# Optimization experiments

Hardware: AMD Instinct MI355X
Metric: run time of the kernel (lower is better)

## Reference

```python
import jax, jax.numpy as jnp
import numpy as np

NEG_INF = -1.0e12  # matches torch's -1000000000000.0 fill


def setup_inputs() -> dict:
    key = jax.random.key(0)
    k1, k2, k3, k4, k5 = jax.random.split(key, 5)
    B, S, H, D = 4, 4096, 1024, 64  # D = hidden_size // num_attention_heads
    x = jax.random.normal(k1, (B, S, H), dtype=jnp.float32)
    mask = jax.random.randint(k2, (B, S), 0, 2, dtype=jnp.int32)
    # nn.Linear(H, D, bias=False) weights have shape [D, H]; y = x @ W.T
    scale = 1.0 / np.sqrt(H)
    Wk = jax.random.normal(k3, (D, H), dtype=jnp.float32) * scale
    Wq = jax.random.normal(k4, (D, H), dtype=jnp.float32) * scale
    Wv = jax.random.normal(k5, (D, H), dtype=jnp.float32) * scale
    return {"x": x, "mask": mask, "Wk": Wk, "Wq": Wq, "Wv": Wv}


def reference(x, mask, Wk, Wq, Wv):
    D = Wk.shape[0]
    scale = 1.0 / jnp.sqrt(jnp.asarray(D, dtype=x.dtype))
    keys = jnp.einsum('bsh,dh->bsd', x, Wk)      # [B,S,D]
    queries = jnp.einsum('bsh,dh->bsd', x, Wq)   # [B,S,D]
    # NOTE: original computes keys @ queries^T (K first), scores[b,i,j] = k_i . q_j
    scores = jnp.einsum('bsd,btd->bst', keys, queries) * scale  # [B,S,S]
    # mask==0 at position p masks COLUMN p of scores (dim=2), matching
    # attention_scores[batch_idx, :, position_idx] = -1e12
    scores = jnp.where((mask == 0)[:, None, :], NEG_INF, scores)
    weights = jax.nn.softmax(scores, axis=2)
    # dropout prob = 0.0 -> identity
    values = jnp.einsum('bsh,dh->bsd', x, Wv)    # [B,S,D]
    hidden_state = jnp.einsum('bst,btd->bsd', weights, values)
    return hidden_state
```

## Files before the change

kernel.cpp:

```cpp
#include <hip/hip_runtime.h>
#include <hip/hip_bf16.h>
#include <math.h>

#define B_ 4
#define S_ 4096
#define H_ 1024
#define D_ 64
#define M_ (B_*S_)
#define NEGINF (-1.0e12f)

typedef __attribute__((ext_vector_type(8))) short bf16x8;
typedef __attribute__((ext_vector_type(8))) unsigned short u16x8;
typedef __attribute__((ext_vector_type(8))) _Float16 f16x8;
typedef __attribute__((ext_vector_type(4))) _Float16 f16x4;
typedef __attribute__((ext_vector_type(4))) float f32x4;

#define OFF_WH   0
#define OFF_WL   393216
#define OFF_KF   786432
#define OFF_QF   2883584
#define OFF_VTF  4980736
#define OFF_PACC 7077888
#define OFF_PM   23855104
#define OFF_PL2  24117248

__device__ __forceinline__ unsigned short f2bf_rne(float f) {
    union { float f; unsigned u; } v; v.f = f;
    unsigned r = (v.u + 0x7fffu + ((v.u >> 16) & 1u)) >> 16;
    return (unsigned short)r;
}
__device__ __forceinline__ float bf2f(unsigned short h) {
    union { unsigned u; float f; } v; v.u = ((unsigned)h) << 16;
    return v.f;
}
__device__ __forceinline__ void split1(float f, unsigned short& h, unsigned short& l) {
    union { float f; unsigned u; } v; v.f = f;
    h = (unsigned short)(v.u >> 16);
    l = f2bf_rne(f - bf2f(h));
}
__device__ __forceinline__ void split8(const float4& a, const float4& b, u16x8& hi, u16x8& lo) {
    float f[8] = {a.x,a.y,a.z,a.w, b.x,b.y,b.z,b.w};
    #pragma unroll
    for (int i = 0; i < 8; ++i) {
        unsigned short h, l; split1(f[i], h, l);
        hi[i] = h; lo[i] = l;
    }
}

__global__ __launch_bounds__(256)
void wconv(const float* __restrict__ Wk, const float* __restrict__ Wq,
           const float* __restrict__ Wv, char* __restrict__ wsb)
{
    short* Wh = (short*)(wsb + OFF_WH);
    short* Wl = (short*)(wsb + OFF_WL);
    const int n = blockIdx.x;
    const int t = threadIdx.x;
    const float* src = (n < 64) ? (Wk + (size_t)n*H_)
                     : (n < 128 ? (Wq + (size_t)(n-64)*H_) : (Wv + (size_t)(n-128)*H_));
    float4 v = *(const float4*)(src + t*4);
    unsigned short h0,l0,h1,l1,h2,l2,h3,l3;
    split1(v.x,h0,l0); split1(v.y,h1,l1); split1(v.z,h2,l2); split1(v.w,h3,l3);
    ushort4 hv; hv.x=h0; hv.y=h1; hv.z=h2; hv.w=h3;
    ushort4 lv; lv.x=l0; lv.y=l1; lv.z=l2; lv.w=l3;
    *(ushort4*)(Wh + n*1024 + t*4) = hv;
    *(ushort4*)(Wl + n*1024 + t*4) = lv;
}

__global__ __launch_bounds__(256, 1)
void qkv_mfma(const float* __restrict__ x, char* __restrict__ wsb)
{
    __shared__ short Ah[4096], Al[4096];
    __shared__ short Bh[12288], Bl[12288];

    const short* __restrict__ Whg = (const short*)(wsb + OFF_WH);
    const short* __restrict__ Wlg = (const short*)(wsb + OFF_WL);
    _Float16* Kf  = (_Float16*)(wsb + OFF_KF);
    _Float16* Qf  = (_Float16*)(wsb + OFF_QF);
    _Float16* Vtf = (_Float16*)(wsb + OFF_VTF);

    const int tid = threadIdx.x;
    const int w = tid >> 6, l = tid & 63;
    const int l15 = l & 15, l4 = l >> 4;
    const int m0 = blockIdx.x * 64;

    const int arow0 = tid >> 3,        ac0 = (tid & 7) * 8;
    const int arow1 = (tid + 256) >> 3;
    const int aoff0 = arow0*64 + (ac0 ^ ((arow0 & 7) << 3));
    const int aoff1 = arow1*64 + (ac0 ^ ((arow1 & 7) << 3));

    float4 xa0, xa1, xa2, xa3;
    u16x8 wbh0, wbh1, wbh2, wbh3, wbh4, wbh5;
    u16x8 wbl0, wbl1, wbl2, wbl3, wbl4, wbl5;

#define QKV_PREFETCH(K0) do {                                                  \
    xa0 = *(const float4*)(x + (size_t)(m0 + arow0)*H_ + (K0) + ac0);          \
    xa1 = *(const float4*)(x + (size_t)(m0 + arow0)*H_ + (K0) + ac0 + 4);      \
    xa2 = *(const float4*)(x + (size_t)(m0 + arow1)*H_ + (K0) + ac0);          \
    xa3 = *(const float4*)(x + (size_t)(m0 + arow1)*H_ + (K0) + ac0 + 4);      \
    { int idx=tid;        int r=idx>>3, c8=(idx&7)*8;                          \
      wbh0 = *(const u16x8*)(Whg + r*1024 + (K0) + c8);                        \
      wbl0 = *(const u16x8*)(Wlg + r*1024 + (K0) + c8); }                      \
    { int idx=tid+256;    int r=idx>>3, c8=(idx&7)*8;                          \
      wbh1 = *(const u16x8*)(Whg + r*1024 + (K0) + c8);                        \
      wbl1 = *(const u16x8*)(Wlg + r*1024 + (K0) + c8); }                      \
    { int idx=tid+512;    int r=idx>>3, c8=(idx&7)*8;                          \
      wbh2 = *(const u16x8*)(Whg + r*1024 + (K0) + c8);                        \
      wbl2 = *(const u16x8*)(Wlg + r*1024 + (K0) + c8); }                      \
    { int idx=tid+768;    int r=idx>>3, c8=(idx&7)*8;                          \
      wbh3 = *(const u16x8*)(Whg + r*1024 + (K0) + c8);                        \
      wbl3 = *(const u16x8*)(Wlg + r*1024 + (K0) + c8); }                      \
    { int idx=tid+1024;   int r=idx>>3, c8=(idx&7)*8;                          \
      wbh4 = *(const u16x8*)(Whg + r*1024 + (K0) + c8);                        \
      wbl4 = *(const u16x8*)(Wlg + r*1024 + (K0) + c8); }                      \
    { int idx=tid+1280;   int r=idx>>3, c8=(idx&7)*8;                          \
      wbh5 = *(const u16x8*)(Whg + r*1024 + (K0) + c8);                        \
      wbl5 = *(const u16x8*)(Wlg + r*1024 + (K0) + c8); }                      \
} while (0)

    QKV_PREFETCH(0);

    f32x4 acc[4][3];
    #pragma unroll
    for (int ms = 0; ms < 4; ++ms)
        #pragma unroll
        for (int nl = 0; nl < 3; ++nl) acc[ms][nl] = (f32x4){0.f,0.f,0.f,0.f};

    for (int k0 = 0; k0 < H_; k0 += 64) {
        __syncthreads();
        {
            u16x8 h, lo8;
            split8(xa0, xa1, h, lo8);
            *(u16x8*)(Ah + aoff0) = h;  *(u16x8*)(Al + aoff0) = lo8;
            split8(xa2, xa3, h, lo8);
            *(u16x8*)(Ah + aoff1) = h;  *(u16x8*)(Al + aoff1) = lo8;
        }
        {
            { int idx=tid;      int r=idx>>3, c8=(idx&7)*8; int off=r*64+(c8^((r&7)<<3));
              *(u16x8*)(Bh+off)=wbh0; *(u16x8*)(Bl+off)=wbl0; }
            { int idx=tid+256;  int r=idx>>3, c8=(idx&7)*8; int off=r*64+(c8^((r&7)<<3));
              *(u16x8*)(Bh+off)=wbh1; *(u16x8*)(Bl+off)=wbl1; }
            { int idx=tid+512;  int r=idx>>3, c8=(idx&7)*8; int off=r*64+(c8^((r&7)<<3));
              *(u16x8*)(Bh+off)=wbh2; *(u16x8*)(Bl+off)=wbl2; }
            { int idx=tid+768;  int r=idx>>3, c8=(idx&7)*8; int off=r*64+(c8^((r&7)<<3));
              *(u16x8*)(Bh+off)=wbh3; *(u16x8*)(Bl+off)=wbl3; }
            { int idx=tid+1024; int r=idx>>3, c8=(idx&7)*8; int off=r*64+(c8^((r&7)<<3));
              *(u16x8*)(Bh+off)=wbh4; *(u16x8*)(Bl+off)=wbl4; }
            { int idx=tid+1280; int r=idx>>3, c8=(idx&7)*8; int off=r*64+(c8^((r&7)<<3));
              *(u16x8*)(Bh+off)=wbh5; *(u16x8*)(Bl+off)=wbl5; }
        }
        int kn = (k0 + 64 < H_) ? k0 + 64 : 0;
        QKV_PREFETCH(kn);
        __syncthreads();

        #pragma unroll
        for (int ks = 0; ks < 2; ++ks) {
            const int cofs = (32*ks + 8*l4) ^ ((l15 & 7) << 3);
            bf16x8 ah[4], al[4];
            #pragma unroll
            for (int ms = 0; ms < 4; ++ms) {
                ah[ms] = *(const bf16x8*)(Ah + (16*ms + l15)*64 + cofs);
                al[ms] = *(const bf16x8*)(Al + (16*ms + l15)*64 + cofs);
            }
            #pragma unroll
            for (int nl = 0; nl < 3; ++nl) {
                const int nrow = (3*w + nl)*16 + l15;
                const int boff = nrow*64 + ((32*ks + 8*l4) ^ ((nrow & 7) << 3));
                bf16x8 bh = *(const bf16x8*)(Bh + boff);
                bf16x8 bl = *(const bf16x8*)(Bl + boff);
                #pragma unroll
                for (int ms = 0; ms < 4; ++ms) {
                    acc[ms][nl] = __builtin_amdgcn_mfma_f32_16x16x32_bf16(ah[ms], bh, acc[ms][nl], 0,0,0);
                    acc[ms][nl] = __builtin_amdgcn_mfma_f32_16x16x32_bf16(ah[ms], bl, acc[ms][nl], 0,0,0);
                    acc[ms][nl] = __builtin_amdgcn_mfma_f32_16x16x32_bf16(al[ms], bh, acc[ms][nl], 0,0,0);
                }
            }
        }
    }

    #pragma unroll
    for (int nl = 0; nl < 3; ++nl) {
        const int nt = 3*w + nl;
        const int n = nt*16 + l15;
        #pragma unroll
        for (int ms = 0; ms < 4; ++ms) {
            if (nt < 4) {
                #pragma unroll
                for (int e = 0; e < 4; ++e)
                    Kf[(size_t)(m0 + 16*ms + 4*l4 + e)*64 + n] = (_Float16)acc[ms][nl][e];
            } else if (nt < 8) {
                #pragma unroll
                for (int e = 0; e < 4; ++e)
                    Qf[(size_t)(m0 + 16*ms + 4*l4 + e)*64 + (n - 64)] = (_Float16)acc[ms][nl][e];
            } else {
                f16x4 pk;
                pk[0] = (_Float16)acc[ms][nl][0]; pk[1] = (_Float16)acc[ms][nl][1];
                pk[2] = (_Float16)acc[ms][nl][2]; pk[3] = (_Float16)acc[ms][nl][3];
                *(f16x4*)(Vtf + (size_t)(n - 128)*M_ + m0 + 16*ms + 4*l4) = pk;
            }
        }
    }
#undef QKV_PREFETCH
}

__global__ __launch_bounds__(256, 4)
void flash_f16(const int* __restrict__ maskp, char* __restrict__ wsb)
{
    __shared__ _Float16 Qs[4096];
    __shared__ _Float16 Vts[4096];
    __shared__ _Float16 Ps[4][1024];

    const _Float16* __restrict__ Kf  = (const _Float16*)(wsb + OFF_KF);
    const _Float16* __restrict__ Qf  = (const _Float16*)(wsb + OFF_QF);
    const _Float16* __restrict__ Vtf = (const _Float16*)(wsb + OFF_VTF);

    const int tid = threadIdx.x;
    const int w = tid >> 6, l = tid & 63;
    const int l15 = l & 15, l4 = l >> 4;
    const int bx = blockIdx.x;
    const int jh = bx & 3, it = (bx >> 2) & 63, b = bx >> 8;
    const int bS = b * S_;
    const int i0m = bS + it*64;
    const int jbase = jh * 1024;

    f16x8 kf0, kf1;
    {
        const size_t row = (size_t)(i0m + 16*w + l15) * 64;
        kf0 = *(const f16x8*)(Kf + row + 8*l4);
        kf1 = *(const f16x8*)(Kf + row + 32 + 8*l4);
    }

    const int jr0 = tid >> 3, jr1 = jr0 + 32;
    const int c0 = (tid & 7) * 8;
    const int sidx0 = jr0*64 + (c0 ^ ((jr0 & 7) << 3));
    const int sidx1 = jr1*64 + (c0 ^ ((jr1 & 7) << 3));

    u16x8 pq0, pq1, pv0, pv1;
    int mp0, mp1, mp2, mp3;

#define FL_PRELOAD(JC) do {                                                    \
    pq0 = *(const u16x8*)(Qf + (size_t)(bS + (JC) + jr0)*64 + c0);             \
    pq1 = *(const u16x8*)(Qf + (size_t)(bS + (JC) + jr1)*64 + c0);             \
    pv0 = *(const u16x8*)(Vtf + (size_t)jr0*M_ + bS + (JC) + c0);              \
    pv1 = *(const u16x8*)(Vtf + (size_t)jr1*M_ + bS + (JC) + c0);              \
    mp0 = maskp[bS + (JC) +      l15];                                         \
    mp1 = maskp[bS + (JC) + 16 + l15];                                         \
    mp2 = maskp[bS + (JC) + 32 + l15];                                         \
    mp3 = maskp[bS + (JC) + 48 + l15];                                         \
} while (0)

    FL_PRELOAD(jbase);

    f32x4 acc_o0 = {0.f,0.f,0.f,0.f}, acc_o1 = {0.f,0.f,0.f,0.f};
    f32x4 acc_o2 = {0.f,0.f,0.f,0.f}, acc_o3 = {0.f,0.f,0.f,0.f};
    float mi[4], li[4];
    #pragma unroll
    for (int e = 0; e < 4; ++e) { mi[e] = -INFINITY; li[e] = 0.f; }

    for (int jc = jbase; jc < jbase + 1024; jc += 64) {
        __syncthreads();
        *(u16x8*)(void*)(Qs + sidx0)  = pq0;  *(u16x8*)(void*)(Qs + sidx1)  = pq1;
        *(u16x8*)(void*)(Vts + sidx0) = pv0;  *(u16x8*)(void*)(Vts + sidx1) = pv1;
        const int mc0 = mp0, mc1 = mp1, mc2 = mp2, mc3 = mp3;
        int jn = jc + 64; if (jn >= jbase + 1024) jn = jbase;
        FL_PRELOAD(jn);
        __syncthreads();

        f32x4 s0 = {0.f,0.f,0.f,0.f}, s1 = {0.f,0.f,0.f,0.f};
        f32x4 s2 = {0.f,0.f,0.f,0.f}, s3 = {0.f,0.f,0.f,0.f};
        __builtin_amdgcn_s_setprio(1);
        #pragma unroll
        for (int ks = 0; ks < 2; ++ks) {
            const f16x8 ka = ks ? kf1 : kf0;
            const int cofs = (32*ks + 8*l4) ^ ((l15 & 7) << 3);
            s0 = __builtin_amdgcn_mfma_f32_16x16x32_f16(ka, *(const f16x8*)(Qs + (0*16 + l15)*64 + cofs), s0, 0,0,0);
            s1 = __builtin_amdgcn_mfma_f32_16x16x32_f16(ka, *(const f16x8*)(Qs + (1*16 + l15)*64 + cofs), s1, 0,0,0);
            s2 = __builtin_amdgcn_mfma_f32_16x16x32_f16(ka, *(const f16x8*)(Qs + (2*16 + l15)*64 + cofs), s2, 0,0,0);
            s3 = __builtin_amdgcn_mfma_f32_16x16x32_f16(ka, *(const f16x8*)(Qs + (3*16 + l15)*64 + cofs), s3, 0,0,0);
        }
        __builtin_amdgcn_s_setprio(0);

        _Float16* pw = &Ps[w][0];
        #pragma unroll
        for (int e = 0; e < 4; ++e) {
            float sv0 = mc0 ? s0[e]*0.125f : NEGINF;
            float sv1 = mc1 ? s1[e]*0.125f : NEGINF;
            float sv2 = mc2 ? s2[e]*0.125f : NEGINF;
            float sv3 = mc3 ? s3[e]*0.125f : NEGINF;
            float rm = fmaxf(fmaxf(sv0, sv1), fmaxf(sv2, sv3));
            rm = fmaxf(rm, __shfl_xor(rm, 1));
            rm = fmaxf(rm, __shfl_xor(rm, 2));
            rm = fmaxf(rm, __shfl_xor(rm, 4));
            rm = fmaxf(rm, __shfl_xor(rm, 8));
            if (__ballot(rm > mi[e])) {
                const float mnew = fmaxf(mi[e], rm);
                const float alpha = __expf(mi[e] - mnew);
                li[e] *= alpha;
                acc_o0[e] *= alpha; acc_o1[e] *= alpha;
                acc_o2[e] *= alpha; acc_o3[e] *= alpha;
                mi[e] = mnew;
            }
            const float p0 = __expf(sv0 - mi[e]);
            const float p1 = __expf(sv1 - mi[e]);
            const float p2 = __expf(sv2 - mi[e]);
            const float p3 = __expf(sv3 - mi[e]);
            float lsum = p0 + p1 + p2 + p3;
            lsum += __shfl_xor(lsum, 1);
            lsum += __shfl_xor(lsum, 2);
            lsum += __shfl_xor(lsum, 4);
            lsum += __shfl_xor(lsum, 8);
            li[e] += lsum;
            const int il = 4*l4 + e;
            const int swz = (il & 7) << 3;
            pw[il*64 + ((     l15) ^ swz)] = (_Float16)p0;
            pw[il*64 + ((16 + l15) ^ swz)] = (_Float16)p1;
            pw[il*64 + ((32 + l15) ^ swz)] = (_Float16)p2;
            pw[il*64 + ((48 + l15) ^ swz)] = (_Float16)p3;
        }

        __builtin_amdgcn_s_setprio(1);
        #pragma unroll
        for (int ks = 0; ks < 2; ++ks) {
            const int cofs = (32*ks + 8*l4) ^ ((l15 & 7) << 3);
            f16x8 pa = *(const f16x8*)(pw + l15*64 + cofs);
            acc_o0 = __builtin_amdgcn_mfma_f32_16x16x32_f16(pa, *(const f16x8*)(Vts + (0*16 + l15)*64 + cofs), acc_o0, 0,0,0);
            acc_o1 = __builtin_amdgcn_mfma_f32_16x16x32_f16(pa, *(const f16x8*)(Vts + (1*16 + l15)*64 + cofs), acc_o1, 0,0,0);
            acc_o2 = __builtin_amdgcn_mfma_f32_16x16x32_f16(pa, *(const f16x8*)(Vts + (2*16 + l15)*64 + cofs), acc_o2, 0,0,0);
            acc_o3 = __builtin_amdgcn_mfma_f32_16x16x32_f16(pa, *(const f16x8*)(Vts + (3*16 + l15)*64 + cofs), acc_o3, 0,0,0);
        }
        __builtin_amdgcn_s_setprio(0);
    }

    float* pacc = (float*)(wsb + OFF_PACC) + (size_t)bx * 4096;
    float* pm   = (float*)(wsb + OFF_PM)  + bx * 64;
    float* pl2  = (float*)(wsb + OFF_PL2) + bx * 64;
    #pragma unroll
    for (int e = 0; e < 4; ++e) {
        const int rowo = (16*w + 4*l4 + e) * 64;
        pacc[rowo +  0 + l15] = acc_o0[e];
        pacc[rowo + 16 + l15] = acc_o1[e];
        pacc[rowo + 32 + l15] = acc_o2[e];
        pacc[rowo + 48 + l15] = acc_o3[e];
    }
    if (l15 == 0) {
        #pragma unroll
        for (int e = 0; e < 4; ++e) {
            pm[16*w + 4*l4 + e]  = mi[e];
            pl2[16*w + 4*l4 + e] = li[e];
        }
    }
#undef FL_PRELOAD
}

__global__ __launch_bounds__(256)
void combine(const char* __restrict__ wsb, float* __restrict__ out)
{
    const float* pacc = (const float*)(wsb + OFF_PACC);
    const float* pm   = (const float*)(wsb + OFF_PM);
    const float* pl   = (const float*)(wsb + OFF_PL2);
    const int gid = blockIdx.x * 256 + threadIdx.x;
    const int row = gid >> 4, q = gid & 15;
    const int b = row >> 12, it = (row >> 6) & 63, il = row & 63;
    const int pb0 = b*256 + it*4;
    float m0 = pm[(pb0+0)*64 + il], m1 = pm[(pb0+1)*64 + il];
    float m2 = pm[(pb0+2)*64 + il], m3 = pm[(pb0+3)*64 + il];
    float l0 = pl[(pb0+0)*64 + il], l1 = pl[(pb0+1)*64 + il];
    float l2 = pl[(pb0+2)*64 + il], l3 = pl[(pb0+3)*64 + il];
    const float M = fmaxf(fmaxf(m0, m1), fmaxf(m2, m3));
    const float w0 = __expf(m0 - M), w1 = __expf(m1 - M);
    const float w2 = __expf(m2 - M), w3 = __expf(m3 - M);
    const float inv = 1.0f / (l0*w0 + l1*w1 + l2*w2 + l3*w3);
    const float4 a0 = *(const float4*)(pacc + (size_t)(pb0+0)*4096 + il*64 + q*4);
    const float4 a1 = *(const float4*)(pacc + (size_t)(pb0+1)*4096 + il*64 + q*4);
    const float4 a2 = *(const float4*)(pacc + (size_t)(pb0+2)*4096 + il*64 + q*4);
    const float4 a3 = *(const float4*)(pacc + (size_t)(pb0+3)*4096 + il*64 + q*4);
    float4 o;
    o.x = (a0.x*w0 + a1.x*w1 + a2.x*w2 + a3.x*w3) * inv;
    o.y = (a0.y*w0 + a1.y*w1 + a2.y*w2 + a3.y*w3) * inv;
    o.z = (a0.z*w0 + a1.z*w1 + a2.z*w2 + a3.z*w3) * inv;
    o.w = (a0.w*w0 + a1.w*w1 + a2.w*w2 + a3.w*w3) * inv;
    *(float4*)(out + (size_t)row*64 + q*4) = o;
}

extern "C" void kernel_launch(void* const* d_in, const int* in_sizes, int n_in,
                              void* d_out, int out_size, void* d_ws, size_t ws_size,
                              hipStream_t stream) {
    const float* x    = (const float*)d_in[0];
    const int*   mask = (const int*)d_in[1];
    const float* Wk   = (const float*)d_in[2];
    const float* Wq   = (const float*)d_in[3];
    const float* Wv   = (const float*)d_in[4];
    float* out = (float*)d_out;
    char*  wsb = (char*)d_ws;

    hipLaunchKernelGGL(wconv,     dim3(192),  dim3(256), 0, stream, Wk, Wq, Wv, wsb);
    hipLaunchKernelGGL(qkv_mfma,  dim3(M_/64),dim3(256), 0, stream, x, wsb);
    hipLaunchKernelGGL(flash_f16, dim3(1024), dim3(256), 0, stream, mask, wsb);
    hipLaunchKernelGGL(combine,   dim3(1024), dim3(256), 0, stream, wsb, out);
}
```

Baseline: 188.6 us.

## Enlarge attention and QKV tiles to 512 threads, transpose scores, lazy softmax rescale

The flash kernel now processes 128 query rows per block with 8 waves, so each staged Q/V chunk in LDS is reused by twice as many rows. The score MFMA operands are swapped so each lane owns one row's statistics; this removes most cross-lane max and sum shuffles and lets the mask load as int4 vectors. The softmax switches to exp2 with log2e folded into the scale, and the accumulator is only rescaled when the running max grows by more than 8. The QKV projection is retiled to 32-row blocks with 8 waves, and the combine kernel is updated for the new partial-result layout. The costs are more registers and LDS per block and possibly lower occupancy.

```diff
diff --git a/kernel.cpp b/kernel.cpp
--- a/kernel.cpp
+++ b/kernel.cpp
@@ -8,6 +8,7 @@
 #define D_ 64
 #define M_ (B_*S_)
 #define NEGINF (-1.0e12f)
+#define LOG2E 1.4426950408889634f
 
 typedef __attribute__((ext_vector_type(8))) short bf16x8;
 typedef __attribute__((ext_vector_type(8))) unsigned short u16x8;
@@ -37,14 +38,6 @@
     union { float f; unsigned u; } v; v.f = f;
     h = (unsigned short)(v.u >> 16);
     l = f2bf_rne(f - bf2f(h));
-}
-__device__ __forceinline__ void split8(const float4& a, const float4& b, u16x8& hi, u16x8& lo) {
-    float f[8] = {a.x,a.y,a.z,a.w, b.x,b.y,b.z,b.w};
-    #pragma unroll
-    for (int i = 0; i < 8; ++i) {
-        unsigned short h, l; split1(f[i], h, l);
-        hi[i] = h; lo[i] = l;
-    }
 }
 
 __global__ __launch_bounds__(256)
@@ -66,11 +59,11 @@
     *(ushort4*)(Wl + n*1024 + t*4) = lv;
 }
 
-__global__ __launch_bounds__(256, 1)
+__global__ __launch_bounds__(512, 4)
 void qkv_mfma(const float* __restrict__ x, char* __restrict__ wsb)
 {
-    __shared__ short Ah[4096], Al[4096];
-    __shared__ short Bh[12288], Bl[12288];
+    __shared__ __align__(16) short Ah[2048], Al[2048];
+    __shared__ __align__(16) short Bh[12288], Bl[12288];
 
     const short* __restrict__ Whg = (const short*)(wsb + OFF_WH);
     const short* __restrict__ Wlg = (const short*)(wsb + OFF_WL);
@@ -81,133 +74,105 @@
     const int tid = threadIdx.x;
     const int w = tid >> 6, l = tid & 63;
     const int l15 = l & 15, l4 = l >> 4;
-    const int m0 = blockIdx.x * 64;
-
-    const int arow0 = tid >> 3,        ac0 = (tid & 7) * 8;
-    const int arow1 = (tid + 256) >> 3;
-    const int aoff0 = arow0*64 + (ac0 ^ ((arow0 & 7) << 3));
-    const int aoff1 = arow1*64 + (ac0 ^ ((arow1 & 7) << 3));
-
-    float4 xa0, xa1, xa2, xa3;
-    u16x8 wbh0, wbh1, wbh2, wbh3, wbh4, wbh5;
-    u16x8 wbl0, wbl1, wbl2, wbl3, wbl4, wbl5;
+    const int wm = w & 1, wn = w >> 1;
+    const int m0 = blockIdx.x * 32;
+
+    const int arow = tid >> 4, ac0 = (tid & 15) * 4;
+    const int aoff = arow*64 + (ac0 ^ ((arow & 7) << 3));
+
+    float4 xa;
+    u16x8 wbh0, wbh1, wbh2, wbl0, wbl1, wbl2;
 
 #define QKV_PREFETCH(K0) do {                                                  \
-    xa0 = *(const float4*)(x + (size_t)(m0 + arow0)*H_ + (K0) + ac0);          \
-    xa1 = *(const float4*)(x + (size_t)(m0 + arow0)*H_ + (K0) + ac0 + 4);      \
-    xa2 = *(const float4*)(x + (size_t)(m0 + arow1)*H_ + (K0) + ac0);          \
-    xa3 = *(const float4*)(x + (size_t)(m0 + arow1)*H_ + (K0) + ac0 + 4);      \
-    { int idx=tid;        int r=idx>>3, c8=(idx&7)*8;                          \
+    xa = *(const float4*)(x + (size_t)(m0 + arow)*H_ + (K0) + ac0);            \
+    { int idx = tid;        int r = idx >> 3, c8 = (idx & 7)*8;                \
       wbh0 = *(const u16x8*)(Whg + r*1024 + (K0) + c8);                        \
       wbl0 = *(const u16x8*)(Wlg + r*1024 + (K0) + c8); }                      \
-    { int idx=tid+256;    int r=idx>>3, c8=(idx&7)*8;                          \
+    { int idx = tid + 512;  int r = idx >> 3, c8 = (idx & 7)*8;                \
       wbh1 = *(const u16x8*)(Whg + r*1024 + (K0) + c8);                        \
       wbl1 = *(const u16x8*)(Wlg + r*1024 + (K0) + c8); }                      \
-    { int idx=tid+512;    int r=idx>>3, c8=(idx&7)*8;                          \
+    { int idx = tid + 1024; int r = idx >> 3, c8 = (idx & 7)*8;                \
       wbh2 = *(const u16x8*)(Whg + r*1024 + (K0) + c8);                        \
       wbl2 = *(const u16x8*)(Wlg + r*1024 + (K0) + c8); }                      \
-    { int idx=tid+768;    int r=idx>>3, c8=(idx&7)*8;                          \
-      wbh3 = *(const u16x8*)(Whg + r*1024 + (K0) + c8);                        \
-      wbl3 = *(const u16x8*)(Wlg + r*1024 + (K0) + c8); }                      \
-    { int idx=tid+1024;   int r=idx>>3, c8=(idx&7)*8;                          \
-      wbh4 = *(const u16x8*)(Whg + r*1024 + (K0) + c8);                        \
-      wbl4 = *(const u16x8*)(Wlg + r*1024 + (K0) + c8); }                      \
-    { int idx=tid+1280;   int r=idx>>3, c8=(idx&7)*8;                          \
-      wbh5 = *(const u16x8*)(Whg + r*1024 + (K0) + c8);                        \
-      wbl5 = *(const u16x8*)(Wlg + r*1024 + (K0) + c8); }                      \
 } while (0)
 
     QKV_PREFETCH(0);
 
-    f32x4 acc[4][3];
-    #pragma unroll
-    for (int ms = 0; ms < 4; ++ms)
-        #pragma unroll
-        for (int nl = 0; nl < 3; ++nl) acc[ms][nl] = (f32x4){0.f,0.f,0.f,0.f};
+    f32x4 acc0 = {0.f,0.f,0.f,0.f}, acc1 = {0.f,0.f,0.f,0.f}, acc2 = {0.f,0.f,0.f,0.f};
 
     for (int k0 = 0; k0 < H_; k0 += 64) {
         __syncthreads();
         {
-            u16x8 h, lo8;
-            split8(xa0, xa1, h, lo8);
-            *(u16x8*)(Ah + aoff0) = h;  *(u16x8*)(Al + aoff0) = lo8;
-            split8(xa2, xa3, h, lo8);
-            *(u16x8*)(Ah + aoff1) = h;  *(u16x8*)(Al + aoff1) = lo8;
+            unsigned short h0,l0,h1,l1,h2,l2,h3,l3;
+            split1(xa.x,h0,l0); split1(xa.y,h1,l1);
+            split1(xa.z,h2,l2); split1(xa.w,h3,l3);
+            ushort4 hv; hv.x=h0; hv.y=h1; hv.z=h2; hv.w=h3;
+            ushort4 lv; lv.x=l0; lv.y=l1; lv.z=l2; lv.w=l3;
+            *(ushort4*)(Ah + aoff) = hv;
+            *(ushort4*)(Al + aoff) = lv;
         }
         {
-            { int idx=tid;      int r=idx>>3, c8=(idx&7)*8; int off=r*64+(c8^((r&7)<<3));
-              *(u16x8*)(Bh+off)=wbh0; *(u16x8*)(Bl+off)=wbl0; }
-            { int idx=tid+256;  int r=idx>>3, c8=(idx&7)*8; int off=r*64+(c8^((r&7)<<3));
-              *(u16x8*)(Bh+off)=wbh1; *(u16x8*)(Bl+off)=wbl1; }
-            { int idx=tid+512;  int r=idx>>3, c8=(idx&7)*8; int off=r*64+(c8^((r&7)<<3));
-              *(u16x8*)(Bh+off)=wbh2; *(u16x8*)(Bl+off)=wbl2; }
-            { int idx=tid+768;  int r=idx>>3, c8=(idx&7)*8; int off=r*64+(c8^((r&7)<<3));
-              *(u16x8*)(Bh+off)=wbh3; *(u16x8*)(Bl+off)=wbl3; }
-            { int idx=tid+1024; int r=idx>>3, c8=(idx&7)*8; int off=r*64+(c8^((r&7)<<3));
-              *(u16x8*)(Bh+off)=wbh4; *(u16x8*)(Bl+off)=wbl4; }
-            { int idx=tid+1280; int r=idx>>3, c8=(idx&7)*8; int off=r*64+(c8^((r&7)<<3));
-              *(u16x8*)(Bh+off)=wbh5; *(u16x8*)(Bl+off)=wbl5; }
+            { int idx = tid;        int r = idx>>3, c8 = (idx&7)*8; int off = r*64 + (c8 ^ ((r&7)<<3));
+              *(u16x8*)(Bh + off) = wbh0; *(u16x8*)(Bl + off) = wbl0; }
+            { int idx = tid + 512;  int r = idx>>3, c8 = (idx&7)*8; int off = r*64 + (c8 ^ ((r&7)<<3));
+              *(u16x8*)(Bh + off) = wbh1; *(u16x8*)(Bl + off) = wbl1; }
+            { int idx = tid + 1024; int r = idx>>3, c8 = (idx&7)*8; int off = r*64 + (c8 ^ ((r&7)<<3));
+              *(u16x8*)(Bh + off) = wbh2; *(u16x8*)(Bl + off) = wbl2; }
         }
         int kn = (k0 + 64 < H_) ? k0 + 64 : 0;
         QKV_PREFETCH(kn);
         __syncthreads();
 
+        __builtin_amdgcn_s_setprio(1);
         #pragma unroll
         for (int ks = 0; ks < 2; ++ks) {
             const int cofs = (32*ks + 8*l4) ^ ((l15 & 7) << 3);
-            bf16x8 ah[4], al[4];
-            #pragma unroll
-            for (int ms = 0; ms < 4; ++ms) {
-                ah[ms] = *(const bf16x8*)(Ah + (16*ms + l15)*64 + cofs);
-                al[ms] = *(const bf16x8*)(Al + (16*ms + l15)*64 + cofs);
-            }
+            const bf16x8 ah = *(const bf16x8*)(Ah + (16*wm + l15)*64 + cofs);
+            const bf16x8 al8 = *(const bf16x8*)(Al + (16*wm + l15)*64 + cofs);
             #pragma unroll
             for (int nl = 0; nl < 3; ++nl) {
-                const int nrow = (3*w + nl)*16 + l15;
+                const int nrow = (3*wn + nl)*16 + l15;
                 const int boff = nrow*64 + ((32*ks + 8*l4) ^ ((nrow & 7) << 3));
-                bf16x8 bh = *(const bf16x8*)(Bh + boff);
-                bf16x8 bl = *(const bf16x8*)(Bl + boff);
-                #pragma unroll
-                for (int ms = 0; ms < 4; ++ms) {
-                    acc[ms][nl] = __builtin_amdgcn_mfma_f32_16x16x32_bf16(ah[ms], bh, acc[ms][nl], 0,0,0);
-                    acc[ms][nl] = __builtin_amdgcn_mfma_f32_16x16x32_bf16(ah[ms], bl, acc[ms][nl], 0,0,0);
-                    acc[ms][nl] = __builtin_amdgcn_mfma_f32_16x16x32_bf16(al[ms], bh, acc[ms][nl], 0,0,0);
-                }
+                const bf16x8 bh = *(const bf16x8*)(Bh + boff);
+                const bf16x8 bl8 = *(const bf16x8*)(Bl + boff);
+                f32x4* ac = (nl == 0) ? &acc0 : ((nl == 1) ? &acc1 : &acc2);
+                *ac = __builtin_amdgcn_mfma_f32_16x16x32_bf16(ah, bh, *ac, 0,0,0);
+                *ac = __builtin_amdgcn_mfma_f32_16x16x32_bf16(ah, bl8, *ac, 0,0,0);
+                *ac = __builtin_amdgcn_mfma_f32_16x16x32_bf16(al8, bh, *ac, 0,0,0);
             }
         }
+        __builtin_amdgcn_s_setprio(0);
     }
 
     #pragma unroll
     for (int nl = 0; nl < 3; ++nl) {
-        const int nt = 3*w + nl;
+        const int nt = 3*wn + nl;
         const int n = nt*16 + l15;
-        #pragma unroll
-        for (int ms = 0; ms < 4; ++ms) {
-            if (nt < 4) {
-                #pragma unroll
-                for (int e = 0; e < 4; ++e)
-                    Kf[(size_t)(m0 + 16*ms + 4*l4 + e)*64 + n] = (_Float16)acc[ms][nl][e];
-            } else if (nt < 8) {
-                #pragma unroll
-                for (int e = 0; e < 4; ++e)
-                    Qf[(size_t)(m0 + 16*ms + 4*l4 + e)*64 + (n - 64)] = (_Float16)acc[ms][nl][e];
-            } else {
-                f16x4 pk;
-                pk[0] = (_Float16)acc[ms][nl][0]; pk[1] = (_Float16)acc[ms][nl][1];
-                pk[2] = (_Float16)acc[ms][nl][2]; pk[3] = (_Float16)acc[ms][nl][3];
-                *(f16x4*)(Vtf + (size_t)(n - 128)*M_ + m0 + 16*ms + 4*l4) = pk;
-            }
+        const f32x4 av = (nl == 0) ? acc0 : ((nl == 1) ? acc1 : acc2);
+        if (nt < 4) {
+            #pragma unroll
+            for (int e = 0; e < 4; ++e)
+                Kf[(size_t)(m0 + 16*wm + 4*l4 + e)*64 + n] = (_Float16)av[e];
+        } else if (nt < 8) {
+            #pragma unroll
+            for (int e = 0; e < 4; ++e)
+                Qf[(size_t)(m0 + 16*wm + 4*l4 + e)*64 + (n - 64)] = (_Float16)av[e];
+        } else {
+            f16x4 pk;
+            pk[0] = (_Float16)av[0]; pk[1] = (_Float16)av[1];
+            pk[2] = (_Float16)av[2]; pk[3] = (_Float16)av[3];
+            *(f16x4*)(Vtf + (size_t)(n - 128)*M_ + m0 + 16*wm + 4*l4) = pk;
         }
     }
 #undef QKV_PREFETCH
 }
 
-__global__ __launch_bounds__(256, 4)
+__global__ __launch_bounds__(512, 4)
 void flash_f16(const int* __restrict__ maskp, char* __restrict__ wsb)
 {
-    __shared__ _Float16 Qs[4096];
-    __shared__ _Float16 Vts[4096];
-    __shared__ _Float16 Ps[4][1024];
+    __shared__ __align__(16) _Float16 Qs[4096];
+    __shared__ __align__(16) _Float16 Vts[4096];
+    __shared__ __align__(16) _Float16 Ps[8][1024];
 
     const _Float16* __restrict__ Kf  = (const _Float16*)(wsb + OFF_KF);
     const _Float16* __restrict__ Qf  = (const _Float16*)(wsb + OFF_QF);
@@ -217,10 +182,11 @@
     const int w = tid >> 6, l = tid & 63;
     const int l15 = l & 15, l4 = l >> 4;
     const int bx = blockIdx.x;
-    const int jh = bx & 3, it = (bx >> 2) & 63, b = bx >> 8;
+    const int jh = bx & 3, it = (bx >> 2) & 31, b = bx >> 7;
     const int bS = b * S_;
-    const int i0m = bS + it*64;
+    const int i0m = bS + it*128;
     const int jbase = jh * 1024;
+    const float SC = 0.125f * LOG2E;
 
     f16x8 kf0, kf1;
     {
@@ -229,126 +195,131 @@
         kf1 = *(const f16x8*)(Kf + row + 32 + 8*l4);
     }
 
-    const int jr0 = tid >> 3, jr1 = jr0 + 32;
+    const int jr = tid >> 3;
     const int c0 = (tid & 7) * 8;
-    const int sidx0 = jr0*64 + (c0 ^ ((jr0 & 7) << 3));
-    const int sidx1 = jr1*64 + (c0 ^ ((jr1 & 7) << 3));
-
-    u16x8 pq0, pq1, pv0, pv1;
-    int mp0, mp1, mp2, mp3;
-
-#define FL_PRELOAD(JC) do {                                                    \
-    pq0 = *(const u16x8*)(Qf + (size_t)(bS + (JC) + jr0)*64 + c0);             \
-    pq1 = *(const u16x8*)(Qf + (size_t)(bS + (JC) + jr1)*64 + c0);             \
-    pv0 = *(const u16x8*)(Vtf + (size_t)jr0*M_ + bS + (JC) + c0);              \
-    pv1 = *(const u16x8*)(Vtf + (size_t)jr1*M_ + bS + (JC) + c0);              \
-    mp0 = maskp[bS + (JC) +      l15];                                         \
-    mp1 = maskp[bS + (JC) + 16 + l15];                                         \
-    mp2 = maskp[bS + (JC) + 32 + l15];                                         \
-    mp3 = maskp[bS + (JC) + 48 + l15];                                         \
+    const int sidx = jr*64 + (c0 ^ ((jr & 7) << 3));
+
+    u16x8 pq, pv;
+    int4 mm0, mm1, mm2, mm3;
+
+#define PRELOAD_QV(JC) do {                                                    \
+    pq = *(const u16x8*)(Qf + (size_t)(bS + (JC) + jr)*64 + c0);               \
+    pv = *(const u16x8*)(Vtf + (size_t)jr*M_ + bS + (JC) + c0);                \
 } while (0)
-
-    FL_PRELOAD(jbase);
-
-    f32x4 acc_o0 = {0.f,0.f,0.f,0.f}, acc_o1 = {0.f,0.f,0.f,0.f};
-    f32x4 acc_o2 = {0.f,0.f,0.f,0.f}, acc_o3 = {0.f,0.f,0.f,0.f};
-    float mi[4], li[4];
-    #pragma unroll
-    for (int e = 0; e < 4; ++e) { mi[e] = -INFINITY; li[e] = 0.f; }
+#define PRELOAD_MK(JC) do {                                                    \
+    mm0 = *(const int4*)(maskp + bS + (JC) +  0 + 4*l4);                       \
+    mm1 = *(const int4*)(maskp + bS + (JC) + 16 + 4*l4);                       \
+    mm2 = *(const int4*)(maskp + bS + (JC) + 32 + 4*l4);                       \
+    mm3 = *(const int4*)(maskp + bS + (JC) + 48 + 4*l4);                       \
+} while (0)
+
+    PRELOAD_QV(jbase);
+    PRELOAD_MK(jbase);
+
+    f32x4 acc0 = {0.f,0.f,0.f,0.f}, acc1 = {0.f,0.f,0.f,0.f};
+    f32x4 acc2 = {0.f,0.f,0.f,0.f}, acc3 = {0.f,0.f,0.f,0.f};
+    float mi = -INFINITY, li = 0.f;
 
     for (int jc = jbase; jc < jbase + 1024; jc += 64) {
         __syncthreads();
-        *(u16x8*)(void*)(Qs + sidx0)  = pq0;  *(u16x8*)(void*)(Qs + sidx1)  = pq1;
-        *(u16x8*)(void*)(Vts + sidx0) = pv0;  *(u16x8*)(void*)(Vts + sidx1) = pv1;
-        const int mc0 = mp0, mc1 = mp1, mc2 = mp2, mc3 = mp3;
+        *(u16x8*)(void*)(Qs + sidx)  = pq;
+        *(u16x8*)(void*)(Vts + sidx) = pv;
+        __syncthreads();
         int jn = jc + 64; if (jn >= jbase + 1024) jn = jbase;
-        FL_PRELOAD(jn);
-        __syncthreads();
-
-        f32x4 s0 = {0.f,0.f,0.f,0.f}, s1 = {0.f,0.f,0.f,0.f};
-        f32x4 s2 = {0.f,0.f,0.f,0.f}, s3 = {0.f,0.f,0.f,0.f};
+        PRELOAD_QV(jn);
+
+        f32x4 sq0 = {0.f,0.f,0.f,0.f}, sq1 = {0.f,0.f,0.f,0.f};
+        f32x4 sq2 = {0.f,0.f,0.f,0.f}, sq3 = {0.f,0.f,0.f,0.f};
         __builtin_amdgcn_s_setprio(1);
         #pragma unroll
         for (int ks = 0; ks < 2; ++ks) {
             const f16x8 ka = ks ? kf1 : kf0;
             const int cofs = (32*ks + 8*l4) ^ ((l15 & 7) << 3);
-            s0 = __builtin_amdgcn_mfma_f32_16x16x32_f16(ka, *(const f16x8*)(Qs + (0*16 + l15)*64 + cofs), s0, 0,0,0);
-            s1 = __builtin_amdgcn_mfma_f32_16x16x32_f16(ka, *(const f16x8*)(Qs + (1*16 + l15)*64 + cofs), s1, 0,0,0);
-            s2 = __builtin_amdgcn_mfma_f32_16x16x32_f16(ka, *(const f16x8*)(Qs + (2*16 + l15)*64 + cofs), s2, 0,0,0);
-            s3 = __builtin_amdgcn_mfma_f32_16x16x32_f16(ka, *(const f16x8*)(Qs + (3*16 + l15)*64 + cofs), s3, 0,0,0);
+            sq0 = __builtin_amdgcn_mfma_f32_16x16x32_f16(*(const f16x8*)(Qs + (0*16 + l15)*64 + cofs), ka, sq0, 0,0,0);
+            sq1 = __builtin_amdgcn_mfma_f32_16x16x32_f16(*(const f16x8*)(Qs + (1*16 + l15)*64 + cofs), ka, sq1, 0,0,0);
+            sq2 = __builtin_amdgcn_mfma_f32_16x16x32_f16(*(const f16x8*)(Qs + (2*16 + l15)*64 + cofs), ka, sq2, 0,0,0);
+            sq3 = __builtin_amdgcn_mfma_f32_16x16x32_f16(*(const f16x8*)(Qs + (3*16 + l15)*64 + cofs), ka, sq3, 0,0,0);
         }
         __builtin_amdgcn_s_setprio(0);
 
+        float sv[16];
+        sv[ 0] = mm0.x ? sq0[0]*SC : NEGINF;  sv[ 1] = mm0.y ? sq0[1]*SC : NEGINF;
+        sv[ 2] = mm0.z ? sq0[2]*SC : NEGINF;  sv[ 3] = mm0.w ? sq0[3]*SC : NEGINF;
+        sv[ 4] = mm1.x ? sq1[0]*SC : NEGINF;  sv[ 5] = mm1.y ? sq1[1]*SC : NEGINF;
+        sv[ 6] = mm1.z ? sq1[2]*SC : NEGINF;  sv[ 7] = mm1.w ? sq1[3]*SC : NEGINF;
+        sv[ 8] = mm2.x ? sq2[0]*SC : NEGINF;  sv[ 9] = mm2.y ? sq2[1]*SC : NEGINF;
+        sv[10] = mm2.z ? sq2[2]*SC : NEGINF;  sv[11] = mm2.w ? sq2[3]*SC : NEGINF;
+        sv[12] = mm3.x ? sq3[0]*SC : NEGINF;  sv[13] = mm3.y ? sq3[1]*SC : NEGINF;
+        sv[14] = mm3.z ? sq3[2]*SC : NEGINF;  sv[15] = mm3.w ? sq3[3]*SC : NEGINF;
+
+        float rm = sv[0];
+        #pragma unroll
+        for (int k = 1; k < 16; ++k) rm = fmaxf(rm, sv[k]);
+        rm = fmaxf(rm, __shfl_xor(rm, 16));
+        rm = fmaxf(rm, __shfl_xor(rm, 32));
+
+        if (__ballot(rm > mi + 8.0f)) {
+            const float mnew = fmaxf(mi, rm);
+            const float alpha = exp2f(mi - mnew);
+            li *= alpha; mi = mnew;
+            const float a0 = __shfl(alpha, 4*l4 + 0);
+            const float a1 = __shfl(alpha, 4*l4 + 1);
+            const float a2 = __shfl(alpha, 4*l4 + 2);
+            const float a3 = __shfl(alpha, 4*l4 + 3);
+            acc0[0]*=a0; acc0[1]*=a1; acc0[2]*=a2; acc0[3]*=a3;
+            acc1[0]*=a0; acc1[1]*=a1; acc1[2]*=a2; acc1[3]*=a3;
+            acc2[0]*=a0; acc2[1]*=a1; acc2[2]*=a2; acc2[3]*=a3;
+            acc3[0]*=a0; acc3[1]*=a1; acc3[2]*=a2; acc3[3]*=a3;
+        }
+
+        float p[16];
+        float sum = 0.f;
+        #pragma unroll
+        for (int k = 0; k < 16; ++k) { p[k] = exp2f(sv[k] - mi); sum += p[k]; }
+        sum += __shfl_xor(sum, 16);
+        sum += __shfl_xor(sum, 32);
+        li += sum;
+
         _Float16* pw = &Ps[w][0];
         #pragma unroll
-        for (int e = 0; e < 4; ++e) {
-            float sv0 = mc0 ? s0[e]*0.125f : NEGINF;
-            float sv1 = mc1 ? s1[e]*0.125f : NEGINF;
-            float sv2 = mc2 ? s2[e]*0.125f : NEGINF;
-            float sv3 = mc3 ? s3[e]*0.125f : NEGINF;
-            float rm = fmaxf(fmaxf(sv0, sv1), fmaxf(sv2, sv3));
-            rm = fmaxf(rm, __shfl_xor(rm, 1));
-            rm = fmaxf(rm, __shfl_xor(rm, 2));
-            rm = fmaxf(rm, __shfl_xor(rm, 4));
-            rm = fmaxf(rm, __shfl_xor(rm, 8));
-            if (__ballot(rm > mi[e])) {
-                const float mnew = fmaxf(mi[e], rm);
-                const float alpha = __expf(mi[e] - mnew);
-                li[e] *= alpha;
-                acc_o0[e] *= alpha; acc_o1[e] *= alpha;
-                acc_o2[e] *= alpha; acc_o3[e] *= alpha;
-                mi[e] = mnew;
-            }
-            const float p0 = __expf(sv0 - mi[e]);
-            const float p1 = __expf(sv1 - mi[e]);
-            const float p2 = __expf(sv2 - mi[e]);
-            const float p3 = __expf(sv3 - mi[e]);
-            float lsum = p0 + p1 + p2 + p3;
-            lsum += __shfl_xor(lsum, 1);
-            lsum += __shfl_xor(lsum, 2);
-            lsum += __shfl_xor(lsum, 4);
-            lsum += __shfl_xor(lsum, 8);
-            li[e] += lsum;
-            const int il = 4*l4 + e;
-            const int swz = (il & 7) << 3;
-            pw[il*64 + ((     l15) ^ swz)] = (_Float16)p0;
-            pw[il*64 + ((16 + l15) ^ swz)] = (_Float16)p1;
-            pw[il*64 + ((32 + l15) ^ swz)] = (_Float16)p2;
-            pw[il*64 + ((48 + l15) ^ swz)] = (_Float16)p3;
-        }
+        for (int mf = 0; mf < 4; ++mf) {
+            f16x4 pk;
+            pk[0] = (_Float16)p[4*mf+0]; pk[1] = (_Float16)p[4*mf+1];
+            pk[2] = (_Float16)p[4*mf+2]; pk[3] = (_Float16)p[4*mf+3];
+            *(f16x4*)(pw + l15*64 + ((16*mf + 4*l4) ^ ((l15 & 7) << 3))) = pk;
+        }
+        PRELOAD_MK(jn);
 
         __builtin_amdgcn_s_setprio(1);
         #pragma unroll
         for (int ks = 0; ks < 2; ++ks) {
             const int cofs = (32*ks + 8*l4) ^ ((l15 & 7) << 3);
-            f16x8 pa = *(const f16x8*)(pw + l15*64 + cofs);
-            acc_o0 = __builtin_amdgcn_mfma_f32_16x16x32_f16(pa, *(const f16x8*)(Vts + (0*16 + l15)*64 + cofs), acc_o0, 0,0,0);
-            acc_o1 = __builtin_amdgcn_mfma_f32_16x16x32_f16(pa, *(const f16x8*)(Vts + (1*16 + l15)*64 + cofs), acc_o1, 0,0,0);
-            acc_o2 = __builtin_amdgcn_mfma_f32_16x16x32_f16(pa, *(const f16x8*)(Vts + (2*16 + l15)*64 + cofs), acc_o2, 0,0,0);
-            acc_o3 = __builtin_amdgcn_mfma_f32_16x16x32_f16(pa, *(const f16x8*)(Vts + (3*16 + l15)*64 + cofs), acc_o3, 0,0,0);
+            const f16x8 pa = *(const f16x8*)(pw + l15*64 + cofs);
+            acc0 = __builtin_amdgcn_mfma_f32_16x16x32_f16(pa, *(const f16x8*)(Vts + (0*16 + l15)*64 + cofs), acc0, 0,0,0);
+            acc1 = __builtin_amdgcn_mfma_f32_16x16x32_f16(pa, *(const f16x8*)(Vts + (1*16 + l15)*64 + cofs), acc1, 0,0,0);
+            acc2 = __builtin_amdgcn_mfma_f32_16x16x32_f16(pa, *(const f16x8*)(Vts + (2*16 + l15)*64 + cofs), acc2, 0,0,0);
+            acc3 = __builtin_amdgcn_mfma_f32_16x16x32_f16(pa, *(const f16x8*)(Vts + (3*16 + l15)*64 + cofs), acc3, 0,0,0);
         }
         __builtin_amdgcn_s_setprio(0);
     }
 
-    float* pacc = (float*)(wsb + OFF_PACC) + (size_t)bx * 4096;
-    float* pm   = (float*)(wsb + OFF_PM)  + bx * 64;
-    float* pl2  = (float*)(wsb + OFF_PL2) + bx * 64;
+    float* pacc = (float*)(wsb + OFF_PACC) + (size_t)bx * 8192;
+    float* pm   = (float*)(wsb + OFF_PM)  + bx * 128;
+    float* pl2  = (float*)(wsb + OFF_PL2) + bx * 128;
     #pragma unroll
     for (int e = 0; e < 4; ++e) {
         const int rowo = (16*w + 4*l4 + e) * 64;
-        pacc[rowo +  0 + l15] = acc_o0[e];
-        pacc[rowo + 16 + l15] = acc_o1[e];
-        pacc[rowo + 32 + l15] = acc_o2[e];
-        pacc[rowo + 48 + l15] = acc_o3[e];
-    }
-    if (l15 == 0) {
-        #pragma unroll
-        for (int e = 0; e < 4; ++e) {
-            pm[16*w + 4*l4 + e]  = mi[e];
-            pl2[16*w + 4*l4 + e] = li[e];
-        }
-    }
-#undef FL_PRELOAD
+        pacc[rowo +  0 + l15] = acc0[e];
+        pacc[rowo + 16 + l15] = acc1[e];
+        pacc[rowo + 32 + l15] = acc2[e];
+        pacc[rowo + 48 + l15] = acc3[e];
+    }
+    if (l4 == 0) {
+        pm[16*w + l15]  = mi;
+        pl2[16*w + l15] = li;
+    }
+#undef PRELOAD_QV
+#undef PRELOAD_MK
 }
 
 __global__ __launch_bounds__(256)
@@ -359,20 +330,21 @@
     const float* pl   = (const float*)(wsb + OFF_PL2);
     const int gid = blockIdx.x * 256 + threadIdx.x;
     const int row = gid >> 4, q = gid & 15;
-    const int b = row >> 12, it = (row >> 6) & 63, il = row & 63;
-    const int pb0 = b*256 + it*4;
-    float m0 = pm[(pb0+0)*64 + il], m1 = pm[(pb0+1)*64 + il];
-    float m2 = pm[(pb0+2)*64 + il], m3 = pm[(pb0+3)*64 + il];
-    float l0 = pl[(pb0+0)*64 + il], l1 = pl[(pb0+1)*64 + il];
-    float l2 = pl[(pb0+2)*64 + il], l3 = pl[(pb0+3)*64 + il];
+    const int b = row >> 12, i = row & 4095;
+    const int it = i >> 7, il = i & 127;
+    const int pb0 = (b << 7) | (it << 2);
+    float m0 = pm[(pb0+0)*128 + il], m1 = pm[(pb0+1)*128 + il];
+    float m2 = pm[(pb0+2)*128 + il], m3 = pm[(pb0+3)*128 + il];
+    float l0 = pl[(pb0+0)*128 + il], l1 = pl[(pb0+1)*128 + il];
+    float l2 = pl[(pb0+2)*128 + il], l3 = pl[(pb0+3)*128 + il];
     const float M = fmaxf(fmaxf(m0, m1), fmaxf(m2, m3));
-    const float w0 = __expf(m0 - M), w1 = __expf(m1 - M);
-    const float w2 = __expf(m2 - M), w3 = __expf(m3 - M);
+    const float w0 = exp2f(m0 - M), w1 = exp2f(m1 - M);
+    const float w2 = exp2f(m2 - M), w3 = exp2f(m3 - M);
     const float inv = 1.0f / (l0*w0 + l1*w1 + l2*w2 + l3*w3);
-    const float4 a0 = *(const float4*)(pacc + (size_t)(pb0+0)*4096 + il*64 + q*4);
-    const float4 a1 = *(const float4*)(pacc + (size_t)(pb0+1)*4096 + il*64 + q*4);
-    const float4 a2 = *(const float4*)(pacc + (size_t)(pb0+2)*4096 + il*64 + q*4);
-    const float4 a3 = *(const float4*)(pacc + (size_t)(pb0+3)*4096 + il*64 + q*4);
+    const float4 a0 = *(const float4*)(pacc + (size_t)(pb0+0)*8192 + il*64 + q*4);
+    const float4 a1 = *(const float4*)(pacc + (size_t)(pb0+1)*8192 + il*64 + q*4);
+    const float4 a2 = *(const float4*)(pacc + (size_t)(pb0+2)*8192 + il*64 + q*4);
+    const float4 a3 = *(const float4*)(pacc + (size_t)(pb0+3)*8192 + il*64 + q*4);
     float4 o;
     o.x = (a0.x*w0 + a1.x*w1 + a2.x*w2 + a3.x*w3) * inv;
     o.y = (a0.y*w0 + a1.y*w1 + a2.y*w2 + a3.y*w3) * inv;
@@ -393,7 +365,7 @@
     char*  wsb = (char*)d_ws;
 
     hipLaunchKernelGGL(wconv,     dim3(192),  dim3(256), 0, stream, Wk, Wq, Wv, wsb);
-    hipLaunchKernelGGL(qkv_mfma,  dim3(M_/64),dim3(256), 0, stream, x, wsb);
-    hipLaunchKernelGGL(flash_f16, dim3(1024), dim3(256), 0, stream, mask, wsb);
+    hipLaunchKernelGGL(qkv_mfma,  dim3(512),  dim3(512), 0, stream, x, wsb);
+    hipLaunchKernelGGL(flash_f16, dim3(512),  dim3(512), 0, stream, mask, wsb);
     hipLaunchKernelGGL(combine,   dim3(1024), dim3(256), 0, stream, wsb, out);
 }
```

Result: faster. 168.6 us (-10.6%).
